# Performance work log

Hardware: AMD Instinct MI355X
Metric: run time of the kernel (lower is better)

The kernel has to match this reference:

```python
import jax, jax.numpy as jnp
import numpy as np
from jax import lax

T, B, D, H, O = 512, 256, 256, 512, 256
MAX_STEPS = 10
EPS = 0.01


def setup_inputs() -> dict:
    key = jax.random.key(0)
    ks = jax.random.split(key, 8)
    ilen = D + 1
    s_ih = 1.0 / np.sqrt(H)

    def xavier(k, shape):
        fan_in, fan_out = shape[1], shape[0]
        lim = np.sqrt(6.0 / (fan_in + fan_out))
        return jax.random.uniform(k, shape, jnp.float32, -lim, lim)

    return {
        "x": jax.random.normal(ks[0], (T, B, D), jnp.float32),
        "W_ih": jax.random.uniform(ks[1], (H, ilen), jnp.float32, -s_ih, s_ih),
        "b_ih": jax.random.uniform(ks[2], (H,), jnp.float32, -s_ih, s_ih),
        "W_hh": jax.random.uniform(ks[3], (H, H), jnp.float32, -s_ih, s_ih),
        "b_hh": jax.random.uniform(ks[4], (H,), jnp.float32, -s_ih, s_ih),
        "W_halt": xavier(ks[5], (1, H)),
        "b_halt": jnp.ones((1,), jnp.float32),  # init.constant_(halt.bias, 1.0)
        "W_out": xavier(ks[6], (O, H)),
        "b_out": jax.random.uniform(ks[7], (O,), jnp.float32, -s_ih, s_ih),
    }


def _act(x, W_ih, b_ih, W_hh, b_hh, W_halt, b_halt, W_out, b_out):
    dt = x.dtype
    Bsz = x.shape[1]

    def time_step(s_t, x_t):
        def ponder(carry, n):
            s, haltsum, running, y_acc, s_acc, steps, rem_tot = carry
            flag = (n == 0).astype(dt)
            # [B, D+1]: input with first-step flag bit
            x_n = jnp.concatenate([x_t, jnp.broadcast_to(flag, (Bsz, 1))], axis=1)
            s_n = jnp.tanh(x_n @ W_ih.T + b_ih + s @ W_hh.T + b_hh)
            h_n = jax.nn.sigmoid(s_n @ W_halt.T + b_halt)[:, 0]
            new_sum = haltsum + h_n
            stopping = (new_sum >= 1.0 - EPS).astype(dt) * running
            still = running - stopping
            remainder = (1.0 - haltsum) * stopping
            p_n = h_n * still + remainder
            y_n = s_n @ W_out.T + b_out
            y_acc = y_acc + y_n * p_n[:, None]
            s_acc = s_acc + s_n * p_n[:, None]
            steps = steps + running
            rem_tot = rem_tot + remainder
            return (s_n, new_sum, still, y_acc, s_acc, steps, rem_tot), None

        init = (
            s_t,
            jnp.zeros((Bsz,), dt),
            jnp.ones((Bsz,), dt),
            jnp.zeros((Bsz, O), dt),
            jnp.zeros((Bsz, H), dt),
            jnp.zeros((Bsz,), dt),
            jnp.zeros((Bsz,), dt),
        )
        (_, _, _, y_acc, s_acc, steps, rem_tot), _ = lax.scan(
            ponder, init, jnp.arange(MAX_STEPS)
        )
        rho = steps + rem_tot
        return s_acc, (y_acc, rho, steps)

    s0 = jnp.zeros((Bsz, H), dt)
    _, (y, rho, n) = lax.scan(time_step, s0, x)
    return y, rho, n


def reference(x, W_ih, b_ih, W_hh, b_hh, W_halt, b_halt, W_out, b_out):
    return _act(x, W_ih, b_ih, W_hh, b_hh, W_halt, b_halt, W_out, b_out)
```

## Files before the change

### kernel.cpp

```cpp
#include <hip/hip_runtime.h>
#include <hip/hip_bf16.h>
#include <cstdint>
#include <cstddef>

#define T_DIM 512
#define B_DIM 256
#define D_DIM 256
#define H_DIM 512
#define O_DIM 256
#define NSTEP 10
#define WIN 16

__device__ __forceinline__ unsigned short f2bf(float f) {
    __hip_bfloat16 b = __float2bfloat16(f);
    return *reinterpret_cast<unsigned short*>(&b);
}

__global__ void k_prep(const float* __restrict__ W_hh,
                       const float* __restrict__ W_ih,
                       const float* __restrict__ W_out,
                       float* __restrict__ whh4,
                       float* __restrict__ wihT,
                       float* __restrict__ woutT)
{
    int idx = blockIdx.x * blockDim.x + threadIdx.x;
    if (idx < 65536) {
        int q = idx >> 9, h = idx & 511;
        ((float4*)whh4)[q * 512 + h] = ((const float4*)W_hh)[h * 128 + q];
    } else if (idx < 65536 + 131072) {
        int j = idx - 65536;
        int d = j >> 9, h = j & 511;
        wihT[d * 512 + h] = W_ih[h * 257 + d];
    } else if (idx < 65536 + 131072 + 131072) {
        int j = idx - (65536 + 131072);
        int h = j >> 8, o = j & 255;
        woutT[h * 256 + o] = W_out[o * 512 + h];
    }
}

__global__ __launch_bounds__(1024, 1) void k_recur11(
    const float* __restrict__ x,
    const float* __restrict__ wihT,
    const float* __restrict__ whh4,
    const float* __restrict__ W_ih,
    const float* __restrict__ w_halt,
    const float* __restrict__ b_ih,
    const float* __restrict__ b_hh,
    const float* __restrict__ b_halt,
    float* out,
    float* __restrict__ psum_g)
{
    __shared__ __align__(16) float sb[2][H_DIM];
    __shared__ __align__(16) float xcw[WIN][H_DIM];
    __shared__ float prt1[H_DIM];
    __shared__ __align__(16) float xst[WIN * D_DIM];
    __shared__ float whalt_l[H_DIM];
    __shared__ float flag_l[H_DIM];
    __shared__ float bias_l[H_DIM];
    __shared__ float red[8];

    const int tid = threadIdx.x;
    const int h = tid & 511;
    const int kh = tid >> 9;
    const int b = blockIdx.x;
    const int wave = tid >> 6;
    const int lane = tid & 63;

    if (!kh) {
        whalt_l[h] = w_halt[h];
        flag_l[h] = W_ih[h * 257 + 256];
        bias_l[h] = b_ih[h] + b_hh[h];
        sb[0][h] = 0.f;
    }

    const float bh = b_halt[0];
    const float THR = 1.0f - 0.01f;
    unsigned short* sacc_out = (unsigned short*)out;
    float* rho_out = out + (size_t)T_DIM * B_DIM * O_DIM;
    float* n_out = rho_out + (size_t)T_DIM * B_DIM;

    const float4* w4 = (const float4*)whh4 + (size_t)kh * 64 * 512 + h;

    int t = 0, nst = 0, cur = 0;
    float hsum = 0.f, runf = 1.f, stepsf = 0.f, remf = 0.f, ps = 0.f;
    float sacc_v = 0.f;

#define DO_REFILL(TB)                                                         \
    {                                                                         \
        __syncthreads();                                                      \
        for (int i = tid; i < WIN * D_DIM; i += 1024)                         \
            xst[i] = x[((size_t)((TB) + (i >> 8)) * B_DIM + b) * D_DIM +      \
                       (i & 255)];                                            \
        __syncthreads();                                                      \
        float xa[8];                                                          \
        _Pragma("unroll") for (int jj = 0; jj < 8; ++jj) xa[jj] = 0.f;        \
        for (int d = 0; d < 256; d += 4) {                                    \
            const float u0 = wihT[(d + 0) * 512 + h];                         \
            const float u1 = wihT[(d + 1) * 512 + h];                         \
            const float u2 = wihT[(d + 2) * 512 + h];                         \
            const float u3 = wihT[(d + 3) * 512 + h];                         \
            _Pragma("unroll") for (int jj = 0; jj < 8; ++jj) {                \
                const float4 xv =                                             \
                    *(const float4*)&xst[(kh * 8 + jj) * 256 + d];            \
                xa[jj] += xv.x * u0;                                          \
                xa[jj] += xv.y * u1;                                          \
                xa[jj] += xv.z * u2;                                          \
                xa[jj] += xv.w * u3;                                          \
            }                                                                 \
        }                                                                     \
        _Pragma("unroll") for (int jj = 0; jj < 8; ++jj)                      \
            xcw[kh * 8 + jj][h] = xa[jj] + bias_l[h];                         \
        __syncthreads();                                                      \
    }

    DO_REFILL(0)

    for (;;) {
        const float4* s4 = (const float4*)&sb[cur][kh << 8];
        float4 A[4];
#pragma unroll
        for (int c = 0; c < 4; ++c) A[c] = float4{0.f, 0.f, 0.f, 0.f};
#pragma unroll 4
        for (int j = 0; j < 64; ++j) {
            const int c = j & 3;
            const float4 wv = w4[(size_t)j * 512];
            const float4 sv = s4[j];
            A[c].x += sv.x * wv.x;
            A[c].y += sv.y * wv.y;
            A[c].z += sv.z * wv.z;
            A[c].w += sv.w * wv.w;
        }
        const float g0 = (A[0].x + A[0].y) + (A[0].z + A[0].w);
        const float g1 = (A[1].x + A[1].y) + (A[1].z + A[1].w);
        const float g2 = (A[2].x + A[2].y) + (A[2].z + A[2].w);
        const float g3 = (A[3].x + A[3].y) + (A[3].z + A[3].w);
        const float pd = (g0 + g1) + (g2 + g3);

        if (kh) prt1[h] = pd;
        __syncthreads();

        float sn = 0.f;
        if (!kh) {
            float base = xcw[t & (WIN - 1)][h];
            if (nst == 0) base += flag_l[h];
            const float pre = (base + pd) + prt1[h];
            sn = tanhf(pre);
            sb[cur ^ 1][h] = sn;
            float pt = sn * whalt_l[h];
#pragma unroll
            for (int m = 1; m < 64; m <<= 1) pt += __shfl_xor(pt, m, 64);
            if (lane == 0) red[wave] = pt;
        }
        __syncthreads();

        const float dotv = ((red[0] + red[1]) + (red[2] + red[3])) +
                           ((red[4] + red[5]) + (red[6] + red[7]));
        const float z = dotv + bh;
        const float hn = 1.f / (1.f + expf(-z));
        const float ns = hsum + hn;
        const float stop = (ns >= THR) ? runf : 0.f;
        const float still = runf - stop;
        const float rem = (1.f - hsum) * stop;
        const float p = hn * still + rem;
        ps += p;
        stepsf += runf;
        remf += rem;
        hsum = ns;
        runf = still;
        nst += 1;
        if (!kh) sacc_v += p * sn;
        cur ^= 1;
        const int adv = (still == 0.f) || (nst == NSTEP);

        if (adv) {
            if (!kh) {
                sb[cur][h] = sacc_v;
                sacc_out[((size_t)t * B_DIM + b) * (size_t)H_DIM + h] =
                    f2bf(sacc_v);
            }
            if (tid == 0) {
                const int bi = t * B_DIM + b;
                psum_g[bi] = ps;
                rho_out[bi] = stepsf + remf;
                n_out[bi] = stepsf;
            }
            hsum = 0.f; runf = 1.f; stepsf = 0.f; remf = 0.f; ps = 0.f;
            nst = 0; sacc_v = 0.f;
            t += 1;
            __syncthreads();
            if (t == T_DIM) break;
            if ((t & (WIN - 1)) == 0) DO_REFILL(t)
        }
    }
#undef DO_REFILL
}

__global__ __launch_bounds__(256) void k_y(
    const float* __restrict__ woutT,
    const float* __restrict__ b_out,
    const float* __restrict__ psum_g,
    float* out)
{
    __shared__ float sl[16][512];
    __shared__ float pl[16];
    const int tid = threadIdx.x;
    const int tb0 = blockIdx.x * 16;
    const unsigned short* sacc = (const unsigned short*)out;
    for (int i = tid; i < 16 * 512; i += 256) {
        unsigned int u = sacc[(size_t)tb0 * 512 + i];
        u <<= 16;
        sl[i >> 9][i & 511] = __uint_as_float(u);
    }
    if (tid < 16) pl[tid] = psum_g[tb0 + tid];
    __syncthreads();
    const int o = tid;
    float acc[16];
#pragma unroll
    for (int r = 0; r < 16; ++r) acc[r] = 0.f;
    for (int hh = 0; hh < 512; hh += 4) {
        const float wv0 = woutT[(hh + 0) * 256 + o];
        const float wv1 = woutT[(hh + 1) * 256 + o];
        const float wv2 = woutT[(hh + 2) * 256 + o];
        const float wv3 = woutT[(hh + 3) * 256 + o];
#pragma unroll
        for (int r = 0; r < 16; ++r) {
            const float4 sv = *(const float4*)&sl[r][hh];
            acc[r] += sv.x * wv0;
            acc[r] += sv.y * wv1;
            acc[r] += sv.z * wv2;
            acc[r] += sv.w * wv3;
        }
    }
    const float bo = b_out[o];
    for (int r = 0; r < 16; ++r)
        out[(size_t)(tb0 + r) * 256 + o] = acc[r] + pl[r] * bo;
}

extern "C" void kernel_launch(void* const* d_in, const int* in_sizes, int n_in,
                              void* d_out, int out_size, void* d_ws, size_t ws_size,
                              hipStream_t stream) {
    const float* x = (const float*)d_in[0];
    const float* W_ih = (const float*)d_in[1];
    const float* b_ih = (const float*)d_in[2];
    const float* W_hh = (const float*)d_in[3];
    const float* b_hh = (const float*)d_in[4];
    const float* W_halt = (const float*)d_in[5];
    const float* b_halt = (const float*)d_in[6];
    const float* W_out = (const float*)d_in[7];
    const float* b_out = (const float*)d_in[8];
    float* out = (float*)d_out;

    char* ws = (char*)d_ws;
    float* whh4 = (float*)ws;
    float* wihT = (float*)(ws + (1u << 20));
    float* woutT = (float*)(ws + (1u << 20) + (512u << 10));
    float* psum = (float*)(ws + (2u << 20));

    hipLaunchKernelGGL(k_prep, dim3(1284), dim3(256), 0, stream,
                       W_hh, W_ih, W_out, whh4, wihT, woutT);
    hipLaunchKernelGGL(k_recur11, dim3(B_DIM), dim3(1024), 0, stream,
                       x, wihT, whh4, W_ih, W_halt, b_ih, b_hh, b_halt,
                       out, psum);
    hipLaunchKernelGGL(k_y, dim3((T_DIM * B_DIM) / 16), dim3(256), 0, stream,
                       woutT, b_out, psum, out);
}
```

Before: 10.48 ms.

## Split recurrent matvec four ways over K and cache part of W_hh in LDS

The W_hh·s matvec in the persistent recurrence kernel is re-partitioned. Each thread now computes two output columns (h and h+256) over a quarter of the K dimension, where before it computed one column over half of K. Four partial-sum rows are reduced through shared memory. The first PFX float4 rows of each even K-quarter's weight slice are preloaded into LDS, which cuts repeated global/L2 weight traffic on every ponder step. In exchange it uses more LDS and more accumulator registers, and the wave work is unbalanced between quarters with and without the LDS prefix.

```diff
diff --git a/kernel.cpp b/kernel.cpp
--- a/kernel.cpp
+++ b/kernel.cpp
@@ -10,6 +10,7 @@
 #define O_DIM 256
 #define NSTEP 10
 #define WIN 16
+#define PFX 5
 
 __device__ __forceinline__ unsigned short f2bf(float f) {
     __hip_bfloat16 b = __float2bfloat16(f);
@@ -38,7 +39,7 @@
     }
 }
 
-__global__ __launch_bounds__(1024, 1) void k_recur11(
+__global__ __launch_bounds__(1024, 1) void k_recur14(
     const float* __restrict__ x,
     const float* __restrict__ wihT,
     const float* __restrict__ whh4,
@@ -50,9 +51,10 @@
     float* out,
     float* __restrict__ psum_g)
 {
+    __shared__ __align__(16) float4 wp_l[2 * PFX * 512];
     __shared__ __align__(16) float sb[2][H_DIM];
     __shared__ __align__(16) float xcw[WIN][H_DIM];
-    __shared__ float prt1[H_DIM];
+    __shared__ float prt[4][H_DIM];
     __shared__ __align__(16) float xst[WIN * D_DIM];
     __shared__ float whalt_l[H_DIM];
     __shared__ float flag_l[H_DIM];
@@ -61,16 +63,23 @@
 
     const int tid = threadIdx.x;
     const int h = tid & 511;
-    const int kh = tid >> 9;
+    const int khr = tid >> 9;
+    const int h2 = tid & 255;
+    const int qk = tid >> 8;
     const int b = blockIdx.x;
     const int wave = tid >> 6;
     const int lane = tid & 63;
 
-    if (!kh) {
-        whalt_l[h] = w_halt[h];
-        flag_l[h] = W_ih[h * 257 + 256];
-        bias_l[h] = b_ih[h] + b_hh[h];
-        sb[0][h] = 0.f;
+    if (tid < 512) {
+        whalt_l[tid] = w_halt[tid];
+        flag_l[tid] = W_ih[tid * 257 + 256];
+        bias_l[tid] = b_ih[tid] + b_hh[tid];
+        sb[0][tid] = 0.f;
+    }
+    for (int i = tid; i < 2 * PFX * 512; i += 1024) {
+        const int kh2 = i / (PFX * 512);
+        const int rem = i - kh2 * (PFX * 512);
+        wp_l[i] = ((const float4*)whh4)[(size_t)kh2 * 64 * 512 + rem];
     }
 
     const float bh = b_halt[0];
@@ -79,7 +88,9 @@
     float* rho_out = out + (size_t)T_DIM * B_DIM * O_DIM;
     float* n_out = rho_out + (size_t)T_DIM * B_DIM;
 
-    const float4* w4 = (const float4*)whh4 + (size_t)kh * 64 * 512 + h;
+    const float4* wL2 = (const float4*)whh4 + (size_t)qk * 32 * 512 + h2;
+    const float4* wpB = &wp_l[(qk >> 1) * PFX * 512 + h2];
+    const bool haspfx = (qk & 1) == 0;
 
     int t = 0, nst = 0, cur = 0;
     float hsum = 0.f, runf = 1.f, stepsf = 0.f, remf = 0.f, ps = 0.f;
@@ -101,7 +112,7 @@
             const float u3 = wihT[(d + 3) * 512 + h];                         \
             _Pragma("unroll") for (int jj = 0; jj < 8; ++jj) {                \
                 const float4 xv =                                             \
-                    *(const float4*)&xst[(kh * 8 + jj) * 256 + d];            \
+                    *(const float4*)&xst[(khr * 8 + jj) * 256 + d];           \
                 xa[jj] += xv.x * u0;                                          \
                 xa[jj] += xv.y * u1;                                          \
                 xa[jj] += xv.z * u2;                                          \
@@ -109,44 +120,77 @@
             }                                                                 \
         }                                                                     \
         _Pragma("unroll") for (int jj = 0; jj < 8; ++jj)                      \
-            xcw[kh * 8 + jj][h] = xa[jj] + bias_l[h];                         \
+            xcw[khr * 8 + jj][h] = xa[jj] + bias_l[h];                        \
         __syncthreads();                                                      \
     }
 
+#define KFMA(WA, WB, i)                                                       \
+    {                                                                         \
+        const int c = (i) & 3;                                                \
+        const float4 sv = s4[(i)];                                            \
+        A[c].x += sv.x * (WA).x; A[c].y += sv.y * (WA).y;                     \
+        A[c].z += sv.z * (WA).z; A[c].w += sv.w * (WA).w;                     \
+        Bc[c].x += sv.x * (WB).x; Bc[c].y += sv.y * (WB).y;                   \
+        Bc[c].z += sv.z * (WB).z; Bc[c].w += sv.w * (WB).w;                   \
+    }
+
     DO_REFILL(0)
 
     for (;;) {
-        const float4* s4 = (const float4*)&sb[cur][kh << 8];
-        float4 A[4];
-#pragma unroll
-        for (int c = 0; c < 4; ++c) A[c] = float4{0.f, 0.f, 0.f, 0.f};
+        const float4* s4 = (const float4*)&sb[cur][qk << 7];
+        float4 A[4], Bc[4];
+#pragma unroll
+        for (int c = 0; c < 4; ++c) {
+            A[c] = float4{0.f, 0.f, 0.f, 0.f};
+            Bc[c] = float4{0.f, 0.f, 0.f, 0.f};
+        }
+        if (haspfx) {
+#pragma unroll
+            for (int i = 0; i < PFX; ++i) {
+                const float4 wvA = wpB[i * 512];
+                const float4 wvB = wpB[i * 512 + 256];
+                KFMA(wvA, wvB, i)
+            }
 #pragma unroll 4
-        for (int j = 0; j < 64; ++j) {
-            const int c = j & 3;
-            const float4 wv = w4[(size_t)j * 512];
-            const float4 sv = s4[j];
-            A[c].x += sv.x * wv.x;
-            A[c].y += sv.y * wv.y;
-            A[c].z += sv.z * wv.z;
-            A[c].w += sv.w * wv.w;
-        }
-        const float g0 = (A[0].x + A[0].y) + (A[0].z + A[0].w);
-        const float g1 = (A[1].x + A[1].y) + (A[1].z + A[1].w);
-        const float g2 = (A[2].x + A[2].y) + (A[2].z + A[2].w);
-        const float g3 = (A[3].x + A[3].y) + (A[3].z + A[3].w);
-        const float pd = (g0 + g1) + (g2 + g3);
-
-        if (kh) prt1[h] = pd;
+            for (int i = PFX; i < 32; ++i) {
+                const float4 wvA = wL2[(size_t)i * 512];
+                const float4 wvB = wL2[(size_t)i * 512 + 256];
+                KFMA(wvA, wvB, i)
+            }
+        } else {
+#pragma unroll 4
+            for (int i = 0; i < 32; ++i) {
+                const float4 wvA = wL2[(size_t)i * 512];
+                const float4 wvB = wL2[(size_t)i * 512 + 256];
+                KFMA(wvA, wvB, i)
+            }
+        }
+        {
+            const float a0 = (A[0].x + A[0].y) + (A[0].z + A[0].w);
+            const float a1 = (A[1].x + A[1].y) + (A[1].z + A[1].w);
+            const float a2 = (A[2].x + A[2].y) + (A[2].z + A[2].w);
+            const float a3 = (A[3].x + A[3].y) + (A[3].z + A[3].w);
+            prt[qk][h2] = (a0 + a1) + (a2 + a3);
+        }
+        {
+            const float a0 = (Bc[0].x + Bc[0].y) + (Bc[0].z + Bc[0].w);
+            const float a1 = (Bc[1].x + Bc[1].y) + (Bc[1].z + Bc[1].w);
+            const float a2 = (Bc[2].x + Bc[2].y) + (Bc[2].z + Bc[2].w);
+            const float a3 = (Bc[3].x + Bc[3].y) + (Bc[3].z + Bc[3].w);
+            prt[qk][h2 + 256] = (a0 + a1) + (a2 + a3);
+        }
         __syncthreads();
 
         float sn = 0.f;
-        if (!kh) {
-            float base = xcw[t & (WIN - 1)][h];
-            if (nst == 0) base += flag_l[h];
-            const float pre = (base + pd) + prt1[h];
+        if (tid < 512) {
+            float base = xcw[t & (WIN - 1)][tid];
+            if (nst == 0) base += flag_l[tid];
+            const float p01 = prt[0][tid] + prt[1][tid];
+            const float p23 = prt[2][tid] + prt[3][tid];
+            const float pre = (base + p01) + p23;
             sn = tanhf(pre);
-            sb[cur ^ 1][h] = sn;
-            float pt = sn * whalt_l[h];
+            sb[cur ^ 1][tid] = sn;
+            float pt = sn * whalt_l[tid];
 #pragma unroll
             for (int m = 1; m < 64; m <<= 1) pt += __shfl_xor(pt, m, 64);
             if (lane == 0) red[wave] = pt;
@@ -168,14 +212,14 @@
         hsum = ns;
         runf = still;
         nst += 1;
-        if (!kh) sacc_v += p * sn;
+        if (tid < 512) sacc_v += p * sn;
         cur ^= 1;
         const int adv = (still == 0.f) || (nst == NSTEP);
 
         if (adv) {
-            if (!kh) {
-                sb[cur][h] = sacc_v;
-                sacc_out[((size_t)t * B_DIM + b) * (size_t)H_DIM + h] =
+            if (tid < 512) {
+                sb[cur][tid] = sacc_v;
+                sacc_out[((size_t)t * B_DIM + b) * (size_t)H_DIM + tid] =
                     f2bf(sacc_v);
             }
             if (tid == 0) {
@@ -193,6 +237,7 @@
         }
     }
 #undef DO_REFILL
+#undef KFMA
 }
 
 __global__ __launch_bounds__(256) void k_y(
@@ -258,7 +303,7 @@
 
     hipLaunchKernelGGL(k_prep, dim3(1284), dim3(256), 0, stream,
                        W_hh, W_ih, W_out, whh4, wihT, woutT);
-    hipLaunchKernelGGL(k_recur11, dim3(B_DIM), dim3(1024), 0, stream,
+    hipLaunchKernelGGL(k_recur14, dim3(B_DIM), dim3(1024), 0, stream,
                        x, wihT, whh4, W_ih, W_halt, b_ih, b_hh, b_halt,
                        out, psum);
     hipLaunchKernelGGL(k_y, dim3((T_DIM * B_DIM) / 16), dim3(256), 0, stream,
```

Result: faster. 9.980 ms, median of 2 (-4.8%).
